# Kernel tuning notes

Measured on AMD Instinct MI355X. Metric: run time of the kernel, lower is better.

Reference implementation:

```python
import jax, jax.numpy as jnp
import numpy as np

N_NODES = 100000
N_EDGES = 3200000
IN_FEAT = 128


def gcn_conv(x, src, dst, W, b, num_nodes):
    # PyG GCNConv: h = x @ W, then symmetric-normalized aggregation with self-loops.
    h = x @ W  # [N, out]
    # add self loops
    loop = jnp.arange(num_nodes, dtype=src.dtype)
    s = jnp.concatenate([src, loop])
    d = jnp.concatenate([dst, loop])
    # degree over destination (col) with unit edge weights
    deg = jax.ops.segment_sum(jnp.ones_like(s, dtype=h.dtype), d, num_segments=num_nodes)
    dinv = jnp.where(deg > 0, jax.lax.rsqrt(deg), 0.0)
    norm = dinv[s] * dinv[d]  # [E+N]
    msg = norm[:, None] * h[s]  # gather source features, scale per edge
    out = jax.ops.segment_sum(msg, d, num_segments=num_nodes)
    return out + b


def setup_inputs() -> dict:
    key = jax.random.key(0)
    ks = jax.random.split(key, 8)
    x = jax.random.normal(ks[0], (N_NODES, IN_FEAT), dtype=jnp.float32)
    edge_index = jax.random.randint(ks[1], (2, N_EDGES), 0, N_NODES, dtype=jnp.int64)
    def glorot(k, shape):
        lim = np.sqrt(6.0 / (shape[0] + shape[1]))
        return jax.random.uniform(k, shape, jnp.float32, -lim, lim)
    return {
        "x": x,
        "edge_index": edge_index,
        "W1": glorot(ks[2], (IN_FEAT, 4)), "b1": jnp.zeros((4,), jnp.float32),
        "W2": glorot(ks[3], (4, 2)),       "b2": jnp.zeros((2,), jnp.float32),
        "W3": glorot(ks[4], (2, 1)),       "b3": jnp.zeros((1,), jnp.float32),
    }


def reference(x, edge_index, W1, b1, W2, b2, W3, b3):
    src, dst = edge_index[0], edge_index[1]
    n = x.shape[0]
    h = gcn_conv(x, src, dst, W1, b1, n)
    h = jax.nn.relu(h)
    # F.dropout(training=self.training): inference mode -> identity
    h = gcn_conv(h, src, dst, W2, b2, n)
    h = jax.nn.relu(h)
    h = gcn_conv(h, src, dst, W3, b3, n)
    return jax.nn.sigmoid(h)  # [N, 1]
```

## Files before the change

### kernel.cpp

```cpp
#include <hip/hip_runtime.h>
#include <hip/hip_bf16.h>
#include <math.h>


#define TPB 256
#define CHUNK 4096
#define EPT (CHUNK / TPB)
#define SLAB2 9216

__global__ __launch_bounds__(TPB) void k_node1(
    const float* __restrict__ x, const float* __restrict__ W1,
    float* __restrict__ hs1, int* __restrict__ cursor, int NB, int n) {
    __shared__ float Ws[512];
    if (blockIdx.x == 0)
        for (int i = threadIdx.x; i < NB; i += TPB) cursor[i] = 0;
    for (int i = threadIdx.x; i < 512; i += TPB) Ws[i] = W1[i];
    __syncthreads();
    int t = blockIdx.x * TPB + threadIdx.x;
    int v = t >> 2, p = t & 3;
    if (v >= n) return;
    const float4* xr = (const float4*)(x + (size_t)v * 128);
    float a0 = 0.f, a1 = 0.f, a2 = 0.f, a3 = 0.f;
#pragma unroll
    for (int i = 0; i < 8; ++i) {
        int c = p + i * 4;
        float4 xx = xr[c];
        const float* w = &Ws[c * 16];
        a0 += xx.x * w[0] + xx.y * w[4] + xx.z * w[8]  + xx.w * w[12];
        a1 += xx.x * w[1] + xx.y * w[5] + xx.z * w[9]  + xx.w * w[13];
        a2 += xx.x * w[2] + xx.y * w[6] + xx.z * w[10] + xx.w * w[14];
        a3 += xx.x * w[3] + xx.y * w[7] + xx.z * w[11] + xx.w * w[15];
    }
    a0 += __shfl_xor(a0, 1); a0 += __shfl_xor(a0, 2);
    a1 += __shfl_xor(a1, 1); a1 += __shfl_xor(a1, 2);
    a2 += __shfl_xor(a2, 1); a2 += __shfl_xor(a2, 2);
    a3 += __shfl_xor(a3, 1); a3 += __shfl_xor(a3, 2);
    if (p == 0) ((float4*)hs1)[v] = make_float4(a0, a1, a2, a3);
}

__global__ __launch_bounds__(TPB) void k_partscatter(
    const int* __restrict__ src, const int* __restrict__ dst,
    int* __restrict__ cursor, unsigned int* __restrict__ pairs2,
    int NB, int E)
{
    __shared__ int hist[512];
    __shared__ int s[TPB];
    __shared__ int gstart[512];
    __shared__ unsigned int sorted[CHUNK];
    int t = threadIdx.x, blk = blockIdx.x;
    int base = blk * CHUNK;
    int n = min(CHUNK, E - base);
    hist[t] = 0; hist[t + 256] = 0;
    __syncthreads();
    unsigned int meta[EPT];
#pragma unroll
    for (int k = 0; k < EPT; ++k) {
        int li = k * TPB + t;
        if (li < n) {
            int d = dst[base + li];
            int lp = atomicAdd(&hist[d >> 8], 1);
            meta[k] = ((unsigned)d << 13) | (unsigned)lp;
        } else meta[k] = 0xFFFFFFFFu;
    }
    __syncthreads();
    int run = 0;
    for (int cb = 0; cb < 512; cb += TPB) {
        int v = hist[cb + t];
        s[t] = v;
        __syncthreads();
        int x = v;
        for (int d = 1; d < TPB; d <<= 1) {
            int y = (t >= d) ? s[t - d] : 0;
            __syncthreads();
            x += y; s[t] = x;
            __syncthreads();
        }
        hist[cb + t] = run + (x - v);
        run += s[TPB - 1];
        __syncthreads();
    }
#pragma unroll
    for (int k = 0; k < EPT; ++k) {
        if (meta[k] != 0xFFFFFFFFu) {
            unsigned m = meta[k];
            int d = (int)(m >> 13);
            int lp = (int)(m & 0x1FFFu);
            unsigned p = (unsigned)src[base + k * TPB + t] | ((unsigned)(d & 255) << 17);
            sorted[hist[d >> 8] + lp] = p;
        }
    }
    __syncthreads();
    for (int b = t; b < NB; b += TPB) {
        int len = hist[b + 1] - hist[b];
        gstart[b] = (len > 0) ? atomicAdd(&cursor[b], len) : 0;
    }
    __syncthreads();
    int grp = t >> 4, ln = t & 15;
    for (int b = grp; b < NB; b += 16) {
        int ls = hist[b];
        int len = hist[b + 1] - ls;
        int gs = gstart[b];
        unsigned int* dp = pairs2 + (size_t)b * SLAB2;
        int lim = min(gs + len, SLAB2);
        for (int k = gs + ln; k < lim; k += 16) dp[k] = sorted[ls + (k - gs)];
    }
}

__global__ __launch_bounds__(TPB) void k_degree2(
    unsigned int* __restrict__ pairs2, const int* __restrict__ cursor,
    int* __restrict__ cnt, int* __restrict__ off, float* __restrict__ dinv,
    float* __restrict__ hs1, int N)
{
    __shared__ unsigned int pl[SLAB2];
    __shared__ int c[TPB], s[TPB], cur[TPB];
    int t = threadIdx.x, b = blockIdx.x;
    int base = b * SLAB2;
    int total = min(cursor[b], SLAB2);
    c[t] = 0;
    __syncthreads();
    for (int i = t; i < total; i += TPB) pl[i] = pairs2[base + i];
    __syncthreads();
    for (int i = t; i < total; i += TPB) atomicAdd(&c[(pl[i] >> 17) & 255], 1);
    __syncthreads();
    int cv = c[t];
    s[t] = cv;
    __syncthreads();
    int x = cv;
    for (int d = 1; d < TPB; d <<= 1) {
        int y = (t >= d) ? s[t - d] : 0;
        __syncthreads();
        x += y; s[t] = x;
        __syncthreads();
    }
    int excl = x - cv;
    int v = (b << 8) + t;
    if (v < N) {
        cnt[v] = cv;
        off[v] = base + excl;
        float di = rsqrtf((float)(cv + 1));
        dinv[v] = di;
        float4 h = ((float4*)hs1)[v];
        ((float4*)hs1)[v] = make_float4(di * h.x, di * h.y, di * h.z, di * h.w);
    }
    cur[t] = excl;
    __syncthreads();
    for (int i = t; i < total; i += TPB) {
        unsigned p = pl[i];
        int pos = atomicAdd(&cur[(p >> 17) & 255], 1);
        pairs2[base + pos] = p & 0x1FFFFu;
    }
}

__global__ __launch_bounds__(TPB) void k_gather1(
    const int* __restrict__ off, const int* __restrict__ cnt,
    const int* __restrict__ ssrc, const float* __restrict__ hs1,
    const float* __restrict__ dinv, const float* __restrict__ b1,
    const float* __restrict__ W2, float* __restrict__ hs2, int n) {
    int t = blockIdx.x * TPB + threadIdx.x;
    int v = t >> 3, p = t & 7;
    if (v >= n) return;
    int base = off[v], c = cnt[v];
    float4 acc = make_float4(0.f, 0.f, 0.f, 0.f);
    for (int i = p; i < c; i += 8) {
        int s = ssrc[base + i];
        float4 h = ((const float4*)hs1)[s];
        acc.x += h.x; acc.y += h.y; acc.z += h.z; acc.w += h.w;
    }
    acc.x += __shfl_xor(acc.x, 1); acc.x += __shfl_xor(acc.x, 2); acc.x += __shfl_xor(acc.x, 4);
    acc.y += __shfl_xor(acc.y, 1); acc.y += __shfl_xor(acc.y, 2); acc.y += __shfl_xor(acc.y, 4);
    acc.z += __shfl_xor(acc.z, 1); acc.z += __shfl_xor(acc.z, 2); acc.z += __shfl_xor(acc.z, 4);
    acc.w += __shfl_xor(acc.w, 1); acc.w += __shfl_xor(acc.w, 2); acc.w += __shfl_xor(acc.w, 4);
    if (p == 0) {
        float4 hv = ((const float4*)hs1)[v];
        float di = dinv[v];
        float o0 = fmaxf(di * (acc.x + hv.x) + b1[0], 0.f);
        float o1 = fmaxf(di * (acc.y + hv.y) + b1[1], 0.f);
        float o2 = fmaxf(di * (acc.z + hv.z) + b1[2], 0.f);
        float o3 = fmaxf(di * (acc.w + hv.w) + b1[3], 0.f);
        float h0 = o0 * W2[0] + o1 * W2[2] + o2 * W2[4] + o3 * W2[6];
        float h1 = o0 * W2[1] + o1 * W2[3] + o2 * W2[5] + o3 * W2[7];
        ((float2*)hs2)[v] = make_float2(di * h0, di * h1);
    }
}

__global__ __launch_bounds__(TPB) void k_gather2(
    const int* __restrict__ off, const int* __restrict__ cnt,
    const int* __restrict__ ssrc, const float* __restrict__ hs2,
    const float* __restrict__ dinv, const float* __restrict__ b2,
    const float* __restrict__ W3, float* __restrict__ hs3, int n) {
    int t = blockIdx.x * TPB + threadIdx.x;
    int v = t >> 3, p = t & 7;
    if (v >= n) return;
    int base = off[v], c = cnt[v];
    float2 acc = make_float2(0.f, 0.f);
    for (int i = p; i < c; i += 8) {
        int s = ssrc[base + i];
        float2 h = ((const float2*)hs2)[s];
        acc.x += h.x; acc.y += h.y;
    }
    acc.x += __shfl_xor(acc.x, 1); acc.x += __shfl_xor(acc.x, 2); acc.x += __shfl_xor(acc.x, 4);
    acc.y += __shfl_xor(acc.y, 1); acc.y += __shfl_xor(acc.y, 2); acc.y += __shfl_xor(acc.y, 4);
    if (p == 0) {
        float2 hv = ((const float2*)hs2)[v];
        float di = dinv[v];
        float o0 = fmaxf(di * (acc.x + hv.x) + b2[0], 0.f);
        float o1 = fmaxf(di * (acc.y + hv.y) + b2[1], 0.f);
        float h3 = o0 * W3[0] + o1 * W3[1];
        hs3[v] = di * h3;
    }
}

__global__ __launch_bounds__(TPB) void k_gather3(
    const int* __restrict__ off, const int* __restrict__ cnt,
    const int* __restrict__ ssrc, const float* __restrict__ hs3,
    const float* __restrict__ dinv, const float* __restrict__ b3,
    float* __restrict__ out, int n) {
    int t = blockIdx.x * TPB + threadIdx.x;
    int v = t >> 3, p = t & 7;
    if (v >= n) return;
    int base = off[v], c = cnt[v];
    float acc = 0.f;
    for (int i = p; i < c; i += 8) acc += hs3[ssrc[base + i]];
    acc += __shfl_xor(acc, 1); acc += __shfl_xor(acc, 2); acc += __shfl_xor(acc, 4);
    if (p == 0) {
        float di = dinv[v];
        float agg = di * (acc + hs3[v]) + b3[0];
        out[v] = 1.0f / (1.0f + __expf(-agg));
    }
}

extern "C" void kernel_launch(void* const* d_in, const int* in_sizes, int n_in,
                              void* d_out, int out_size, void* d_ws, size_t ws_size,
                              hipStream_t stream) {
    const float* x  = (const float*)d_in[0];
    const int* ei   = (const int*)d_in[1];
    const float* W1 = (const float*)d_in[2];
    const float* b1 = (const float*)d_in[3];
    const float* W2 = (const float*)d_in[4];
    const float* b2 = (const float*)d_in[5];
    const float* W3 = (const float*)d_in[6];
    const float* b3 = (const float*)d_in[7];
    float* out = (float*)d_out;

    const int N = in_sizes[0] / 128;
    const int E = in_sizes[1] / 2;
    const int* src = ei;
    const int* dst = ei + E;

    const int NS = (E + CHUNK - 1) / CHUNK;
    const int NB = (N + 255) >> 8;

    char* w = (char*)d_ws;
    auto carve = [&](size_t bytes) { char* p = w; w += (bytes + 15) & ~(size_t)15; return p; };
    unsigned int* pairs2 = (unsigned int*)carve((size_t)NB * SLAB2 * 4);
    int* cursor          = (int*)carve((size_t)NB * 4);
    int* cnt             = (int*)carve((size_t)N * 4);
    int* off             = (int*)carve((size_t)N * 4);
    float* dinv          = (float*)carve((size_t)N * 4);
    float* hs1           = (float*)carve((size_t)N * 16);
    float* hs2           = (float*)carve((size_t)N * 8);
    float* hs3           = (float*)carve((size_t)N * 4);

    const int nbN4 = (4 * N + TPB - 1) / TPB;
    const int nbN8 = (8 * N + TPB - 1) / TPB;

    k_node1      <<<nbN4, TPB, 0, stream>>>(x, W1, hs1, cursor, NB, N);
    k_partscatter<<<NS, TPB, 0, stream>>>(src, dst, cursor, pairs2, NB, E);
    k_degree2    <<<NB, TPB, 0, stream>>>(pairs2, cursor, cnt, off, dinv, hs1, N);
    k_gather1    <<<nbN8, TPB, 0, stream>>>(off, cnt, (const int*)pairs2, hs1, dinv, b1, W2, hs2, N);
    k_gather2    <<<nbN8, TPB, 0, stream>>>(off, cnt, (const int*)pairs2, hs2, dinv, b2, W3, hs3, N);
    k_gather3    <<<nbN8, TPB, 0, stream>>>(off, cnt, (const int*)pairs2, hs3, dinv, b3, out, N);
}
```

Measured before the change: 224.1 us.

## Use per-wave privatized histograms and wave shuffle scans in partition and degree kernels

Replaces the barrier-heavy shared-memory Hillis-Steele scans in the partition-scatter and degree kernels with wavefront shuffle scans plus a small cross-wave combine. Histograms are privatized per wavefront to cut LDS atomic contention. Each wave gets its own sub-offsets, so the scatter stays correct. The edge chunk size is halved to 2048, which doubles the number of scatter blocks and global cursor atomics. The copy-out now uses 4 lanes per bucket instead of 16, giving shorter but less coalesced writes.

```diff
diff --git a/kernel.cpp b/kernel.cpp
--- a/kernel.cpp
+++ b/kernel.cpp
@@ -4,9 +4,18 @@
 
 
 #define TPB 256
-#define CHUNK 4096
+#define CHUNK 2048
 #define EPT (CHUNK / TPB)
 #define SLAB2 9216
+
+__device__ __forceinline__ int wave_incl_scan(int v, int lane) {
+#pragma unroll
+    for (int d = 1; d < 64; d <<= 1) {
+        int y = __shfl_up(v, d);
+        if (lane >= d) v += y;
+    }
+    return v;
+}
 
 __global__ __launch_bounds__(TPB) void k_node1(
     const float* __restrict__ x, const float* __restrict__ W1,
@@ -43,14 +52,19 @@
     int* __restrict__ cursor, unsigned int* __restrict__ pairs2,
     int NB, int E)
 {
-    __shared__ int hist[512];
-    __shared__ int s[TPB];
+    __shared__ int hist4[4 * 512];
+    __shared__ int sstart[513];
     __shared__ int gstart[512];
     __shared__ unsigned int sorted[CHUNK];
+    __shared__ int wtot[4];
     int t = threadIdx.x, blk = blockIdx.x;
+    int lane = t & 63, w = t >> 6;
     int base = blk * CHUNK;
     int n = min(CHUNK, E - base);
-    hist[t] = 0; hist[t + 256] = 0;
+#pragma unroll
+    for (int i = 0; i < 4; ++i) hist4[i * 512 + t] = 0;
+    hist4[0 * 512 + 256 + t] = 0; hist4[1 * 512 + 256 + t] = 0;
+    hist4[2 * 512 + 256 + t] = 0; hist4[3 * 512 + 256 + t] = 0;
     __syncthreads();
     unsigned int meta[EPT];
 #pragma unroll
@@ -58,27 +72,39 @@
         int li = k * TPB + t;
         if (li < n) {
             int d = dst[base + li];
-            int lp = atomicAdd(&hist[d >> 8], 1);
+            int lp = atomicAdd(&hist4[(w << 9) + (d >> 8)], 1);
             meta[k] = ((unsigned)d << 13) | (unsigned)lp;
         } else meta[k] = 0xFFFFFFFFu;
     }
     __syncthreads();
-    int run = 0;
-    for (int cb = 0; cb < 512; cb += TPB) {
-        int v = hist[cb + t];
-        s[t] = v;
+    {
+        int bA = 2 * t, bB = 2 * t + 1;
+        int a0 = hist4[0 * 512 + bA], a1 = hist4[1 * 512 + bA];
+        int a2 = hist4[2 * 512 + bA], a3 = hist4[3 * 512 + bA];
+        int b0 = hist4[0 * 512 + bB], b1 = hist4[1 * 512 + bB];
+        int b2 = hist4[2 * 512 + bB], b3 = hist4[3 * 512 + bB];
+        int totA = a0 + a1 + a2 + a3, totB = b0 + b1 + b2 + b3;
+        int p = totA + totB;
+        int ip = wave_incl_scan(p, lane);
+        if (lane == 63) wtot[w] = ip;
         __syncthreads();
-        int x = v;
-        for (int d = 1; d < TPB; d <<= 1) {
-            int y = (t >= d) ? s[t - d] : 0;
-            __syncthreads();
-            x += y; s[t] = x;
-            __syncthreads();
-        }
-        hist[cb + t] = run + (x - v);
-        run += s[TPB - 1];
-        __syncthreads();
-    }
+        int woff = 0;
+#pragma unroll
+        for (int i = 0; i < 4; ++i) { int wt = wtot[i]; if (i < w) woff += wt; }
+        int exclA = woff + ip - p;
+        int exclB = exclA + totA;
+        sstart[bA] = exclA; sstart[bB] = exclB;
+        hist4[0 * 512 + bA] = exclA;
+        hist4[1 * 512 + bA] = exclA + a0;
+        hist4[2 * 512 + bA] = exclA + a0 + a1;
+        hist4[3 * 512 + bA] = exclA + a0 + a1 + a2;
+        hist4[0 * 512 + bB] = exclB;
+        hist4[1 * 512 + bB] = exclB + b0;
+        hist4[2 * 512 + bB] = exclB + b0 + b1;
+        hist4[3 * 512 + bB] = exclB + b0 + b1 + b2;
+        if (t == 0) sstart[512] = n;
+    }
+    __syncthreads();
 #pragma unroll
     for (int k = 0; k < EPT; ++k) {
         if (meta[k] != 0xFFFFFFFFu) {
@@ -86,23 +112,22 @@
             int d = (int)(m >> 13);
             int lp = (int)(m & 0x1FFFu);
             unsigned p = (unsigned)src[base + k * TPB + t] | ((unsigned)(d & 255) << 17);
-            sorted[hist[d >> 8] + lp] = p;
+            sorted[hist4[(w << 9) + (d >> 8)] + lp] = p;
         }
     }
-    __syncthreads();
     for (int b = t; b < NB; b += TPB) {
-        int len = hist[b + 1] - hist[b];
+        int len = sstart[b + 1] - sstart[b];
         gstart[b] = (len > 0) ? atomicAdd(&cursor[b], len) : 0;
     }
     __syncthreads();
-    int grp = t >> 4, ln = t & 15;
-    for (int b = grp; b < NB; b += 16) {
-        int ls = hist[b];
-        int len = hist[b + 1] - ls;
+    int grp = t >> 2, ln = t & 3;
+    for (int b = grp; b < NB; b += 64) {
+        int ls = sstart[b];
+        int len = sstart[b + 1] - ls;
         int gs = gstart[b];
         unsigned int* dp = pairs2 + (size_t)b * SLAB2;
         int lim = min(gs + len, SLAB2);
-        for (int k = gs + ln; k < lim; k += 16) dp[k] = sorted[ls + (k - gs)];
+        for (int k = gs + ln; k < lim; k += 4) dp[k] = sorted[ls + (k - gs)];
     }
 }
 
@@ -112,27 +137,30 @@
     float* __restrict__ hs1, int N)
 {
     __shared__ unsigned int pl[SLAB2];
-    __shared__ int c[TPB], s[TPB], cur[TPB];
+    __shared__ int c4[4 * 256];
+    __shared__ int wtot[4];
     int t = threadIdx.x, b = blockIdx.x;
+    int lane = t & 63, w = t >> 6;
     int base = b * SLAB2;
     int total = min(cursor[b], SLAB2);
-    c[t] = 0;
+#pragma unroll
+    for (int i = 0; i < 4; ++i) c4[i * 256 + t] = 0;
     __syncthreads();
     for (int i = t; i < total; i += TPB) pl[i] = pairs2[base + i];
     __syncthreads();
-    for (int i = t; i < total; i += TPB) atomicAdd(&c[(pl[i] >> 17) & 255], 1);
-    __syncthreads();
-    int cv = c[t];
-    s[t] = cv;
-    __syncthreads();
-    int x = cv;
-    for (int d = 1; d < TPB; d <<= 1) {
-        int y = (t >= d) ? s[t - d] : 0;
-        __syncthreads();
-        x += y; s[t] = x;
-        __syncthreads();
-    }
-    int excl = x - cv;
+    for (int i = t; i < total; i += TPB)
+        atomicAdd(&c4[(w << 8) + ((pl[i] >> 17) & 255)], 1);
+    __syncthreads();
+    int c0 = c4[0 * 256 + t], c1 = c4[1 * 256 + t];
+    int c2 = c4[2 * 256 + t], c3 = c4[3 * 256 + t];
+    int cv = c0 + c1 + c2 + c3;
+    int ip = wave_incl_scan(cv, lane);
+    if (lane == 63) wtot[w] = ip;
+    __syncthreads();
+    int woff = 0;
+#pragma unroll
+    for (int i = 0; i < 4; ++i) { int wt = wtot[i]; if (i < w) woff += wt; }
+    int excl = woff + ip - cv;
     int v = (b << 8) + t;
     if (v < N) {
         cnt[v] = cv;
@@ -142,11 +170,14 @@
         float4 h = ((float4*)hs1)[v];
         ((float4*)hs1)[v] = make_float4(di * h.x, di * h.y, di * h.z, di * h.w);
     }
-    cur[t] = excl;
+    c4[0 * 256 + t] = excl;
+    c4[1 * 256 + t] = excl + c0;
+    c4[2 * 256 + t] = excl + c0 + c1;
+    c4[3 * 256 + t] = excl + c0 + c1 + c2;
     __syncthreads();
     for (int i = t; i < total; i += TPB) {
         unsigned p = pl[i];
-        int pos = atomicAdd(&cur[(p >> 17) & 255], 1);
+        int pos = atomicAdd(&c4[(w << 8) + ((p >> 17) & 255)], 1);
         pairs2[base + pos] = p & 0x1FFFFu;
     }
 }
```

Result: slower. 235.9 us (+5.3%).

## Fuse all stages into one cooperative persistent kernel with grid syncs

Applied to the files above, without the earlier changes.

Replaces six separate kernel launches with a single cooperative kernel that uses grid-wide syncs between phases. It runs the edge partition-scatter concurrently with the node feature projection by splitting blocks between the two tasks. The degree phase now reads pairs straight from global memory instead of staging a shared slab, and it writes to a separate ssrc buffer. The intent is to remove launch gaps and overlap the independent first stages. In exchange the grid is limited to resident blocks, occupancy may drop because of the large shared union, and grid syncs add their own cost.

```diff
diff --git a/kernel.cpp b/kernel.cpp
--- a/kernel.cpp
+++ b/kernel.cpp
@@ -1,6 +1,9 @@
 #include <hip/hip_runtime.h>
 #include <hip/hip_bf16.h>
+#include <hip/hip_cooperative_groups.h>
 #include <math.h>
+
+namespace cg = cooperative_groups;
 
 
 #define TPB 256
@@ -8,224 +11,215 @@
 #define EPT (CHUNK / TPB)
 #define SLAB2 9216
 
-__global__ __launch_bounds__(TPB) void k_node1(
-    const float* __restrict__ x, const float* __restrict__ W1,
-    float* __restrict__ hs1, int* __restrict__ cursor, int NB, int n) {
-    __shared__ float Ws[512];
-    if (blockIdx.x == 0)
-        for (int i = threadIdx.x; i < NB; i += TPB) cursor[i] = 0;
-    for (int i = threadIdx.x; i < 512; i += TPB) Ws[i] = W1[i];
-    __syncthreads();
-    int t = blockIdx.x * TPB + threadIdx.x;
-    int v = t >> 2, p = t & 3;
-    if (v >= n) return;
-    const float4* xr = (const float4*)(x + (size_t)v * 128);
-    float a0 = 0.f, a1 = 0.f, a2 = 0.f, a3 = 0.f;
+struct Prm {
+    const float* x; const int* src; const int* dst;
+    const float* W1; const float* b1; const float* W2; const float* b2;
+    const float* W3; const float* b3;
+    unsigned int* pairs2; int* cursor; int* ssrc;
+    int* cnt; int* off; float* dinv;
+    float* hs1; float* hs2; float* hs3; float* out;
+    int N, E, NS, NB, psB;
+};
+
+union SH {
+    struct { int hist[512]; int s[TPB]; int gstart[512]; unsigned int sorted[CHUNK]; } ps;
+    struct { int c[TPB]; int s[TPB]; int cur[TPB]; } dg;
+    float Ws[512];
+};
+
+__global__ __launch_bounds__(TPB) void k_mega(Prm p) {
+    cg::grid_group grid = cg::this_grid();
+    __shared__ SH sh;
+    int t = threadIdx.x;
+
+    if ((int)blockIdx.x < p.psB) {
+        for (int blk = blockIdx.x; blk < p.NS; blk += p.psB) {
+            __syncthreads();
+            int base = blk * CHUNK;
+            int n = min(CHUNK, p.E - base);
+            sh.ps.hist[t] = 0; sh.ps.hist[t + 256] = 0;
+            __syncthreads();
+            unsigned int meta[EPT];
 #pragma unroll
-    for (int i = 0; i < 8; ++i) {
-        int c = p + i * 4;
-        float4 xx = xr[c];
-        const float* w = &Ws[c * 16];
-        a0 += xx.x * w[0] + xx.y * w[4] + xx.z * w[8]  + xx.w * w[12];
-        a1 += xx.x * w[1] + xx.y * w[5] + xx.z * w[9]  + xx.w * w[13];
-        a2 += xx.x * w[2] + xx.y * w[6] + xx.z * w[10] + xx.w * w[14];
-        a3 += xx.x * w[3] + xx.y * w[7] + xx.z * w[11] + xx.w * w[15];
-    }
-    a0 += __shfl_xor(a0, 1); a0 += __shfl_xor(a0, 2);
-    a1 += __shfl_xor(a1, 1); a1 += __shfl_xor(a1, 2);
-    a2 += __shfl_xor(a2, 1); a2 += __shfl_xor(a2, 2);
-    a3 += __shfl_xor(a3, 1); a3 += __shfl_xor(a3, 2);
-    if (p == 0) ((float4*)hs1)[v] = make_float4(a0, a1, a2, a3);
-}
-
-__global__ __launch_bounds__(TPB) void k_partscatter(
-    const int* __restrict__ src, const int* __restrict__ dst,
-    int* __restrict__ cursor, unsigned int* __restrict__ pairs2,
-    int NB, int E)
-{
-    __shared__ int hist[512];
-    __shared__ int s[TPB];
-    __shared__ int gstart[512];
-    __shared__ unsigned int sorted[CHUNK];
-    int t = threadIdx.x, blk = blockIdx.x;
-    int base = blk * CHUNK;
-    int n = min(CHUNK, E - base);
-    hist[t] = 0; hist[t + 256] = 0;
-    __syncthreads();
-    unsigned int meta[EPT];
+            for (int k = 0; k < EPT; ++k) {
+                int li = k * TPB + t;
+                if (li < n) {
+                    int d = p.dst[base + li];
+                    int lp = atomicAdd(&sh.ps.hist[d >> 8], 1);
+                    meta[k] = ((unsigned)d << 13) | (unsigned)lp;
+                } else meta[k] = 0xFFFFFFFFu;
+            }
+            __syncthreads();
+            int run = 0;
+            for (int cb = 0; cb < 512; cb += TPB) {
+                int v = sh.ps.hist[cb + t];
+                sh.ps.s[t] = v;
+                __syncthreads();
+                int x = v;
+                for (int d = 1; d < TPB; d <<= 1) {
+                    int y = (t >= d) ? sh.ps.s[t - d] : 0;
+                    __syncthreads();
+                    x += y; sh.ps.s[t] = x;
+                    __syncthreads();
+                }
+                sh.ps.hist[cb + t] = run + (x - v);
+                run += sh.ps.s[TPB - 1];
+                __syncthreads();
+            }
 #pragma unroll
-    for (int k = 0; k < EPT; ++k) {
-        int li = k * TPB + t;
-        if (li < n) {
-            int d = dst[base + li];
-            int lp = atomicAdd(&hist[d >> 8], 1);
-            meta[k] = ((unsigned)d << 13) | (unsigned)lp;
-        } else meta[k] = 0xFFFFFFFFu;
-    }
-    __syncthreads();
-    int run = 0;
-    for (int cb = 0; cb < 512; cb += TPB) {
-        int v = hist[cb + t];
-        s[t] = v;
-        __syncthreads();
-        int x = v;
+            for (int k = 0; k < EPT; ++k) {
+                if (meta[k] != 0xFFFFFFFFu) {
+                    unsigned m = meta[k];
+                    int d = (int)(m >> 13);
+                    int lp = (int)(m & 0x1FFFu);
+                    unsigned pk = (unsigned)p.src[base + k * TPB + t] |
+                                  ((unsigned)(d & 255) << 17);
+                    sh.ps.sorted[sh.ps.hist[d >> 8] + lp] = pk;
+                }
+            }
+            for (int b = t; b < p.NB; b += TPB) {
+                int len = sh.ps.hist[b + 1] - sh.ps.hist[b];
+                sh.ps.gstart[b] = (len > 0) ? atomicAdd(&p.cursor[b], len) : 0;
+            }
+            __syncthreads();
+            int grp = t >> 4, ln = t & 15;
+            for (int b = grp; b < p.NB; b += 16) {
+                int ls = sh.ps.hist[b];
+                int len = sh.ps.hist[b + 1] - ls;
+                int gs = sh.ps.gstart[b];
+                unsigned int* dp = p.pairs2 + (size_t)b * SLAB2;
+                int lim = min(gs + len, SLAB2);
+                for (int k = gs + ln; k < lim; k += 16)
+                    dp[k] = sh.ps.sorted[ls + (k - gs)];
+            }
+        }
+    } else {
+        for (int i = t; i < 512; i += TPB) sh.Ws[i] = p.W1[i];
+        __syncthreads();
+        int nb = gridDim.x - p.psB;
+        for (int tt = ((int)blockIdx.x - p.psB) * TPB + t; tt < 4 * p.N;
+             tt += nb * TPB) {
+            int v = tt >> 2, q = tt & 3;
+            const float4* xr = (const float4*)(p.x + (size_t)v * 128);
+            float a0 = 0.f, a1 = 0.f, a2 = 0.f, a3 = 0.f;
+#pragma unroll
+            for (int i = 0; i < 8; ++i) {
+                int c = q + i * 4;
+                float4 xx = xr[c];
+                const float* w = &sh.Ws[c * 16];
+                a0 += xx.x * w[0] + xx.y * w[4] + xx.z * w[8]  + xx.w * w[12];
+                a1 += xx.x * w[1] + xx.y * w[5] + xx.z * w[9]  + xx.w * w[13];
+                a2 += xx.x * w[2] + xx.y * w[6] + xx.z * w[10] + xx.w * w[14];
+                a3 += xx.x * w[3] + xx.y * w[7] + xx.z * w[11] + xx.w * w[15];
+            }
+            a0 += __shfl_xor(a0, 1); a0 += __shfl_xor(a0, 2);
+            a1 += __shfl_xor(a1, 1); a1 += __shfl_xor(a1, 2);
+            a2 += __shfl_xor(a2, 1); a2 += __shfl_xor(a2, 2);
+            a3 += __shfl_xor(a3, 1); a3 += __shfl_xor(a3, 2);
+            if (q == 0) ((float4*)p.hs1)[v] = make_float4(a0, a1, a2, a3);
+        }
+    }
+    grid.sync();
+
+    for (int b = blockIdx.x; b < p.NB; b += gridDim.x) {
+        __syncthreads();
+        sh.dg.c[t] = 0;
+        __syncthreads();
+        int base = b * SLAB2;
+        int total = min(p.cursor[b], SLAB2);
+        for (int i = t; i < total; i += TPB)
+            atomicAdd(&sh.dg.c[(p.pairs2[base + i] >> 17) & 255], 1);
+        __syncthreads();
+        int cv = sh.dg.c[t];
+        sh.dg.s[t] = cv;
+        __syncthreads();
+        int x = cv;
         for (int d = 1; d < TPB; d <<= 1) {
-            int y = (t >= d) ? s[t - d] : 0;
-            __syncthreads();
-            x += y; s[t] = x;
-            __syncthreads();
-        }
-        hist[cb + t] = run + (x - v);
-        run += s[TPB - 1];
-        __syncthreads();
-    }
-#pragma unroll
-    for (int k = 0; k < EPT; ++k) {
-        if (meta[k] != 0xFFFFFFFFu) {
-            unsigned m = meta[k];
-            int d = (int)(m >> 13);
-            int lp = (int)(m & 0x1FFFu);
-            unsigned p = (unsigned)src[base + k * TPB + t] | ((unsigned)(d & 255) << 17);
-            sorted[hist[d >> 8] + lp] = p;
-        }
-    }
-    __syncthreads();
-    for (int b = t; b < NB; b += TPB) {
-        int len = hist[b + 1] - hist[b];
-        gstart[b] = (len > 0) ? atomicAdd(&cursor[b], len) : 0;
-    }
-    __syncthreads();
-    int grp = t >> 4, ln = t & 15;
-    for (int b = grp; b < NB; b += 16) {
-        int ls = hist[b];
-        int len = hist[b + 1] - ls;
-        int gs = gstart[b];
-        unsigned int* dp = pairs2 + (size_t)b * SLAB2;
-        int lim = min(gs + len, SLAB2);
-        for (int k = gs + ln; k < lim; k += 16) dp[k] = sorted[ls + (k - gs)];
-    }
-}
-
-__global__ __launch_bounds__(TPB) void k_degree2(
-    unsigned int* __restrict__ pairs2, const int* __restrict__ cursor,
-    int* __restrict__ cnt, int* __restrict__ off, float* __restrict__ dinv,
-    float* __restrict__ hs1, int N)
-{
-    __shared__ unsigned int pl[SLAB2];
-    __shared__ int c[TPB], s[TPB], cur[TPB];
-    int t = threadIdx.x, b = blockIdx.x;
-    int base = b * SLAB2;
-    int total = min(cursor[b], SLAB2);
-    c[t] = 0;
-    __syncthreads();
-    for (int i = t; i < total; i += TPB) pl[i] = pairs2[base + i];
-    __syncthreads();
-    for (int i = t; i < total; i += TPB) atomicAdd(&c[(pl[i] >> 17) & 255], 1);
-    __syncthreads();
-    int cv = c[t];
-    s[t] = cv;
-    __syncthreads();
-    int x = cv;
-    for (int d = 1; d < TPB; d <<= 1) {
-        int y = (t >= d) ? s[t - d] : 0;
-        __syncthreads();
-        x += y; s[t] = x;
-        __syncthreads();
-    }
-    int excl = x - cv;
-    int v = (b << 8) + t;
-    if (v < N) {
-        cnt[v] = cv;
-        off[v] = base + excl;
-        float di = rsqrtf((float)(cv + 1));
-        dinv[v] = di;
-        float4 h = ((float4*)hs1)[v];
-        ((float4*)hs1)[v] = make_float4(di * h.x, di * h.y, di * h.z, di * h.w);
-    }
-    cur[t] = excl;
-    __syncthreads();
-    for (int i = t; i < total; i += TPB) {
-        unsigned p = pl[i];
-        int pos = atomicAdd(&cur[(p >> 17) & 255], 1);
-        pairs2[base + pos] = p & 0x1FFFFu;
-    }
-}
-
-__global__ __launch_bounds__(TPB) void k_gather1(
-    const int* __restrict__ off, const int* __restrict__ cnt,
-    const int* __restrict__ ssrc, const float* __restrict__ hs1,
-    const float* __restrict__ dinv, const float* __restrict__ b1,
-    const float* __restrict__ W2, float* __restrict__ hs2, int n) {
-    int t = blockIdx.x * TPB + threadIdx.x;
-    int v = t >> 3, p = t & 7;
-    if (v >= n) return;
-    int base = off[v], c = cnt[v];
-    float4 acc = make_float4(0.f, 0.f, 0.f, 0.f);
-    for (int i = p; i < c; i += 8) {
-        int s = ssrc[base + i];
-        float4 h = ((const float4*)hs1)[s];
-        acc.x += h.x; acc.y += h.y; acc.z += h.z; acc.w += h.w;
-    }
-    acc.x += __shfl_xor(acc.x, 1); acc.x += __shfl_xor(acc.x, 2); acc.x += __shfl_xor(acc.x, 4);
-    acc.y += __shfl_xor(acc.y, 1); acc.y += __shfl_xor(acc.y, 2); acc.y += __shfl_xor(acc.y, 4);
-    acc.z += __shfl_xor(acc.z, 1); acc.z += __shfl_xor(acc.z, 2); acc.z += __shfl_xor(acc.z, 4);
-    acc.w += __shfl_xor(acc.w, 1); acc.w += __shfl_xor(acc.w, 2); acc.w += __shfl_xor(acc.w, 4);
-    if (p == 0) {
-        float4 hv = ((const float4*)hs1)[v];
-        float di = dinv[v];
-        float o0 = fmaxf(di * (acc.x + hv.x) + b1[0], 0.f);
-        float o1 = fmaxf(di * (acc.y + hv.y) + b1[1], 0.f);
-        float o2 = fmaxf(di * (acc.z + hv.z) + b1[2], 0.f);
-        float o3 = fmaxf(di * (acc.w + hv.w) + b1[3], 0.f);
-        float h0 = o0 * W2[0] + o1 * W2[2] + o2 * W2[4] + o3 * W2[6];
-        float h1 = o0 * W2[1] + o1 * W2[3] + o2 * W2[5] + o3 * W2[7];
-        ((float2*)hs2)[v] = make_float2(di * h0, di * h1);
-    }
-}
-
-__global__ __launch_bounds__(TPB) void k_gather2(
-    const int* __restrict__ off, const int* __restrict__ cnt,
-    const int* __restrict__ ssrc, const float* __restrict__ hs2,
-    const float* __restrict__ dinv, const float* __restrict__ b2,
-    const float* __restrict__ W3, float* __restrict__ hs3, int n) {
-    int t = blockIdx.x * TPB + threadIdx.x;
-    int v = t >> 3, p = t & 7;
-    if (v >= n) return;
-    int base = off[v], c = cnt[v];
-    float2 acc = make_float2(0.f, 0.f);
-    for (int i = p; i < c; i += 8) {
-        int s = ssrc[base + i];
-        float2 h = ((const float2*)hs2)[s];
-        acc.x += h.x; acc.y += h.y;
-    }
-    acc.x += __shfl_xor(acc.x, 1); acc.x += __shfl_xor(acc.x, 2); acc.x += __shfl_xor(acc.x, 4);
-    acc.y += __shfl_xor(acc.y, 1); acc.y += __shfl_xor(acc.y, 2); acc.y += __shfl_xor(acc.y, 4);
-    if (p == 0) {
-        float2 hv = ((const float2*)hs2)[v];
-        float di = dinv[v];
-        float o0 = fmaxf(di * (acc.x + hv.x) + b2[0], 0.f);
-        float o1 = fmaxf(di * (acc.y + hv.y) + b2[1], 0.f);
-        float h3 = o0 * W3[0] + o1 * W3[1];
-        hs3[v] = di * h3;
-    }
-}
-
-__global__ __launch_bounds__(TPB) void k_gather3(
-    const int* __restrict__ off, const int* __restrict__ cnt,
-    const int* __restrict__ ssrc, const float* __restrict__ hs3,
-    const float* __restrict__ dinv, const float* __restrict__ b3,
-    float* __restrict__ out, int n) {
-    int t = blockIdx.x * TPB + threadIdx.x;
-    int v = t >> 3, p = t & 7;
-    if (v >= n) return;
-    int base = off[v], c = cnt[v];
-    float acc = 0.f;
-    for (int i = p; i < c; i += 8) acc += hs3[ssrc[base + i]];
-    acc += __shfl_xor(acc, 1); acc += __shfl_xor(acc, 2); acc += __shfl_xor(acc, 4);
-    if (p == 0) {
-        float di = dinv[v];
-        float agg = di * (acc + hs3[v]) + b3[0];
-        out[v] = 1.0f / (1.0f + __expf(-agg));
+            int y = (t >= d) ? sh.dg.s[t - d] : 0;
+            __syncthreads();
+            x += y; sh.dg.s[t] = x;
+            __syncthreads();
+        }
+        int excl = x - cv;
+        int v = (b << 8) + t;
+        if (v < p.N) {
+            p.cnt[v] = cv;
+            p.off[v] = base + excl;
+            float di = rsqrtf((float)(cv + 1));
+            p.dinv[v] = di;
+            float4 h = ((float4*)p.hs1)[v];
+            ((float4*)p.hs1)[v] = make_float4(di * h.x, di * h.y, di * h.z, di * h.w);
+        }
+        sh.dg.cur[t] = excl;
+        __syncthreads();
+        for (int i = t; i < total; i += TPB) {
+            unsigned pp = p.pairs2[base + i];
+            int pos = atomicAdd(&sh.dg.cur[(pp >> 17) & 255], 1);
+            p.ssrc[base + pos] = (int)(pp & 0x1FFFFu);
+        }
+    }
+    grid.sync();
+
+    for (int tt = blockIdx.x * TPB + t; tt < 8 * p.N; tt += gridDim.x * TPB) {
+        int v = tt >> 3, q = tt & 7;
+        int base = p.off[v], c = p.cnt[v];
+        float4 acc = make_float4(0.f, 0.f, 0.f, 0.f);
+        for (int i = q; i < c; i += 8) {
+            int s = p.ssrc[base + i];
+            float4 h = ((const float4*)p.hs1)[s];
+            acc.x += h.x; acc.y += h.y; acc.z += h.z; acc.w += h.w;
+        }
+        acc.x += __shfl_xor(acc.x, 1); acc.x += __shfl_xor(acc.x, 2); acc.x += __shfl_xor(acc.x, 4);
+        acc.y += __shfl_xor(acc.y, 1); acc.y += __shfl_xor(acc.y, 2); acc.y += __shfl_xor(acc.y, 4);
+        acc.z += __shfl_xor(acc.z, 1); acc.z += __shfl_xor(acc.z, 2); acc.z += __shfl_xor(acc.z, 4);
+        acc.w += __shfl_xor(acc.w, 1); acc.w += __shfl_xor(acc.w, 2); acc.w += __shfl_xor(acc.w, 4);
+        if (q == 0) {
+            float4 hv = ((const float4*)p.hs1)[v];
+            float di = p.dinv[v];
+            float o0 = fmaxf(di * (acc.x + hv.x) + p.b1[0], 0.f);
+            float o1 = fmaxf(di * (acc.y + hv.y) + p.b1[1], 0.f);
+            float o2 = fmaxf(di * (acc.z + hv.z) + p.b1[2], 0.f);
+            float o3 = fmaxf(di * (acc.w + hv.w) + p.b1[3], 0.f);
+            float h0 = o0 * p.W2[0] + o1 * p.W2[2] + o2 * p.W2[4] + o3 * p.W2[6];
+            float h1 = o0 * p.W2[1] + o1 * p.W2[3] + o2 * p.W2[5] + o3 * p.W2[7];
+            ((float2*)p.hs2)[v] = make_float2(di * h0, di * h1);
+        }
+    }
+    grid.sync();
+
+    for (int tt = blockIdx.x * TPB + t; tt < 8 * p.N; tt += gridDim.x * TPB) {
+        int v = tt >> 3, q = tt & 7;
+        int base = p.off[v], c = p.cnt[v];
+        float2 acc = make_float2(0.f, 0.f);
+        for (int i = q; i < c; i += 8) {
+            int s = p.ssrc[base + i];
+            float2 h = ((const float2*)p.hs2)[s];
+            acc.x += h.x; acc.y += h.y;
+        }
+        acc.x += __shfl_xor(acc.x, 1); acc.x += __shfl_xor(acc.x, 2); acc.x += __shfl_xor(acc.x, 4);
+        acc.y += __shfl_xor(acc.y, 1); acc.y += __shfl_xor(acc.y, 2); acc.y += __shfl_xor(acc.y, 4);
+        if (q == 0) {
+            float2 hv = ((const float2*)p.hs2)[v];
+            float di = p.dinv[v];
+            float o0 = fmaxf(di * (acc.x + hv.x) + p.b2[0], 0.f);
+            float o1 = fmaxf(di * (acc.y + hv.y) + p.b2[1], 0.f);
+            float h3 = o0 * p.W3[0] + o1 * p.W3[1];
+            p.hs3[v] = di * h3;
+        }
+    }
+    grid.sync();
+
+    for (int tt = blockIdx.x * TPB + t; tt < 8 * p.N; tt += gridDim.x * TPB) {
+        int v = tt >> 3, q = tt & 7;
+        int base = p.off[v], c = p.cnt[v];
+        float acc = 0.f;
+        for (int i = q; i < c; i += 8) acc += p.hs3[p.ssrc[base + i]];
+        acc += __shfl_xor(acc, 1); acc += __shfl_xor(acc, 2); acc += __shfl_xor(acc, 4);
+        if (q == 0) {
+            float di = p.dinv[v];
+            float agg = di * (acc + p.hs3[v]) + p.b3[0];
+            p.out[v] = 1.0f / (1.0f + __expf(-agg));
+        }
     }
 }
 
@@ -234,25 +228,17 @@
                               hipStream_t stream) {
     const float* x  = (const float*)d_in[0];
     const int* ei   = (const int*)d_in[1];
-    const float* W1 = (const float*)d_in[2];
-    const float* b1 = (const float*)d_in[3];
-    const float* W2 = (const float*)d_in[4];
-    const float* b2 = (const float*)d_in[5];
-    const float* W3 = (const float*)d_in[6];
-    const float* b3 = (const float*)d_in[7];
-    float* out = (float*)d_out;
 
     const int N = in_sizes[0] / 128;
     const int E = in_sizes[1] / 2;
-    const int* src = ei;
-    const int* dst = ei + E;
 
     const int NS = (E + CHUNK - 1) / CHUNK;
     const int NB = (N + 255) >> 8;
 
     char* w = (char*)d_ws;
-    auto carve = [&](size_t bytes) { char* p = w; w += (bytes + 15) & ~(size_t)15; return p; };
+    auto carve = [&](size_t bytes) { char* q = w; w += (bytes + 15) & ~(size_t)15; return q; };
     unsigned int* pairs2 = (unsigned int*)carve((size_t)NB * SLAB2 * 4);
+    int* ssrc            = (int*)carve((size_t)NB * SLAB2 * 4);
     int* cursor          = (int*)carve((size_t)NB * 4);
     int* cnt             = (int*)carve((size_t)N * 4);
     int* off             = (int*)carve((size_t)N * 4);
@@ -261,13 +247,29 @@
     float* hs2           = (float*)carve((size_t)N * 8);
     float* hs3           = (float*)carve((size_t)N * 4);
 
-    const int nbN4 = (4 * N + TPB - 1) / TPB;
-    const int nbN8 = (8 * N + TPB - 1) / TPB;
-
-    k_node1      <<<nbN4, TPB, 0, stream>>>(x, W1, hs1, cursor, NB, N);
-    k_partscatter<<<NS, TPB, 0, stream>>>(src, dst, cursor, pairs2, NB, E);
-    k_degree2    <<<NB, TPB, 0, stream>>>(pairs2, cursor, cnt, off, dinv, hs1, N);
-    k_gather1    <<<nbN8, TPB, 0, stream>>>(off, cnt, (const int*)pairs2, hs1, dinv, b1, W2, hs2, N);
-    k_gather2    <<<nbN8, TPB, 0, stream>>>(off, cnt, (const int*)pairs2, hs2, dinv, b2, W3, hs3, N);
-    k_gather3    <<<nbN8, TPB, 0, stream>>>(off, cnt, (const int*)pairs2, hs3, dinv, b3, out, N);
+    int numCU = 256, maxB = 0;
+    hipDeviceGetAttribute(&numCU, hipDeviceAttributeMultiprocessorCount, 0);
+    hipOccupancyMaxActiveBlocksPerMultiprocessor(&maxB, k_mega, TPB, 0);
+    if (maxB < 1) maxB = 1;
+    int grid = numCU * maxB;
+    if (grid < 8) grid = 8;
+
+    int psB = (grid * 3) / 4;
+    if (psB > NS) psB = NS;
+    if (psB >= grid) psB = grid - 1;
+    if (psB < 1) psB = 1;
+
+    Prm prm;
+    prm.x = x; prm.src = ei; prm.dst = ei + E;
+    prm.W1 = (const float*)d_in[2]; prm.b1 = (const float*)d_in[3];
+    prm.W2 = (const float*)d_in[4]; prm.b2 = (const float*)d_in[5];
+    prm.W3 = (const float*)d_in[6]; prm.b3 = (const float*)d_in[7];
+    prm.pairs2 = pairs2; prm.cursor = cursor; prm.ssrc = ssrc;
+    prm.cnt = cnt; prm.off = off; prm.dinv = dinv;
+    prm.hs1 = hs1; prm.hs2 = hs2; prm.hs3 = hs3; prm.out = (float*)d_out;
+    prm.N = N; prm.E = E; prm.NS = NS; prm.NB = NB; prm.psB = psB;
+
+    hipMemsetAsync(cursor, 0, (size_t)NB * 4, stream);
+    void* args[] = { &prm };
+    hipLaunchCooperativeKernel((void*)k_mega, dim3(grid), dim3(TPB), args, 0, stream);
 }
```

Measured after the change: 479.4 us. +113.9%, slower.
